# Kernel optimization log

Measured on AMD Instinct MI355X. Metric: run time of the kernel, lower is better.

The kernel has to match this reference:

```python
import jax, jax.numpy as jnp
import numpy as np

B, T, IN, H, C = 64, 4096, 128, 256, 128


def setup_inputs() -> dict:
    key = jax.random.key(0)
    ks = jax.random.split(key, 7)
    s_ih = 1.0 / np.sqrt(H)
    return {
        "x": jax.random.normal(ks[0], (B, T, IN), dtype=jnp.float32),
        "W_ih": jax.random.uniform(ks[1], (4 * H, IN), jnp.float32, -s_ih, s_ih),
        "W_hh": jax.random.uniform(ks[2], (4 * H, H), jnp.float32, -s_ih, s_ih),
        "b_ih": jax.random.uniform(ks[3], (4 * H,), jnp.float32, -s_ih, s_ih),
        "b_hh": jax.random.uniform(ks[4], (4 * H,), jnp.float32, -s_ih, s_ih),
        "fc_w": jax.random.uniform(ks[5], (C, H), jnp.float32, -s_ih, s_ih),
        "fc_b": jax.random.uniform(ks[6], (C,), jnp.float32, -s_ih, s_ih),
    }


def lstm_cell(x_t, h, c, W_ih, W_hh, b_ih, b_hh):
    # gates: [B, 4H] in PyTorch order i, f, g, o
    gates = x_t @ W_ih.T + b_ih + h @ W_hh.T + b_hh
    i, f, g, o = jnp.split(gates, 4, axis=-1)
    i = jax.nn.sigmoid(i)
    f = jax.nn.sigmoid(f)
    g = jnp.tanh(g)
    o = jax.nn.sigmoid(o)
    c_new = f * c + i * g
    h_new = o * jnp.tanh(c_new)
    return h_new, c_new


def reference(x, W_ih, W_hh, b_ih, b_hh, fc_w, fc_b):
    # Precompute input projections for all timesteps in one big GEMM.
    x_proj = jnp.einsum('bti,gi->tbg', x, W_ih) + b_ih  # [T, B, 4H]

    def step(carry, xp_t):
        h, c = carry
        # truncate_length=1: the torch code detaches (h, c) at EVERY step.
        # Forward math is unaffected by detach.
        h = jax.lax.stop_gradient(h)
        c = jax.lax.stop_gradient(c)
        gates = xp_t + h @ W_hh.T + b_hh
        i, f, g, o = jnp.split(gates, 4, axis=-1)
        c_new = jax.nn.sigmoid(f) * c + jax.nn.sigmoid(i) * jnp.tanh(g)
        h_new = jax.nn.sigmoid(o) * jnp.tanh(c_new)
        return (h_new, c_new), None

    h0 = jnp.zeros((x.shape[0], W_hh.shape[1]), dtype=x.dtype)
    c0 = jnp.zeros_like(h0)
    (h_t, _), _ = jax.lax.scan(step, (h0, c0), x_proj)
    return h_t @ fc_w.T + fc_b
```

## Files before the change

kernel.cpp:

```cpp
#include <hip/hip_runtime.h>

#define B_ 64
#define T_ 4096
#define IN_ 128
#define H_ 256
#define TPB 512

using u64 = unsigned long long;

static constexpr size_t HB2_BYTES = 2ull * B_ * H_ * sizeof(u64);

__device__ __forceinline__ float rdlane_f(float v, int k) {
    return __builtin_bit_cast(float, __builtin_amdgcn_readlane(__builtin_bit_cast(int, v), k));
}
__device__ __forceinline__ float fast_rcp(float x) { return __builtin_amdgcn_rcpf(x); }
__device__ __forceinline__ float fast_sigmoid(float x) {
    return fast_rcp(1.0f + __expf(-x));
}
__device__ __forceinline__ float fast_tanh(float x) {
    float ax = fabsf(x);
    float e  = __expf(-2.0f * ax);
    float t  = (1.0f - e) * fast_rcp(1.0f + e);
    return copysignf(t, x);
}
__device__ __forceinline__ u64 ld_agent(const u64* p) {
    return __hip_atomic_load(p, __ATOMIC_RELAXED, __HIP_MEMORY_SCOPE_AGENT);
}
__device__ __forceinline__ void st_agent(u64* p, u64 v) {
    __hip_atomic_store(p, v, __ATOMIC_RELAXED, __HIP_MEMORY_SCOPE_AGENT);
}

__global__ __launch_bounds__(TPB, 2) void lstm_persist(
    const float* __restrict__ x,
    const float* __restrict__ W_ih,
    const float* __restrict__ W_hh,
    const float* __restrict__ b_ih,
    const float* __restrict__ b_hh,
    const float* __restrict__ fc_w,
    const float* __restrict__ fc_b,
    float* __restrict__ out,
    u64* hb2)
{
    const int blk  = blockIdx.x;
    const int xcd  = blk & 7;
    const int m    = blk >> 3;
    const int s    = m & 3;
    const int b    = ((m >> 2) << 3) | xcd;
    const int tid  = threadIdx.x;
    const int lane = tid & 63;
    const int wave = tid >> 6;
    const int chunk = wave & 3;
    const int sub   = wave >> 2;
    const bool is_upd = (wave == s);

    const int row_base = s * 64 + lane;
    const int k_hh = chunk * 64 + sub * 32;
    const int k_ih = chunk * 32 + sub * 16;

    float w_hh[4][32];
    #pragma unroll
    for (int g = 0; g < 4; ++g) {
        const float4* src = (const float4*)(W_hh + (size_t)(g * 256 + row_base) * H_ + k_hh);
        #pragma unroll
        for (int q = 0; q < 8; ++q) {
            const float4 v = src[q];
            w_hh[g][q*4+0] = v.x; w_hh[g][q*4+1] = v.y;
            w_hh[g][q*4+2] = v.z; w_hh[g][q*4+3] = v.w;
        }
    }
    float w_ih[4][16];
    #pragma unroll
    for (int g = 0; g < 4; ++g) {
        const float4* src = (const float4*)(W_ih + (size_t)(g * 256 + row_base) * IN_ + k_ih);
        #pragma unroll
        for (int q = 0; q < 4; ++q) {
            const float4 v = src[q];
            w_ih[g][q*4+0] = v.x; w_ih[g][q*4+1] = v.y;
            w_ih[g][q*4+2] = v.z; w_ih[g][q*4+3] = v.w;
        }
    }
    float bias_[4] = {0.f, 0.f, 0.f, 0.f};
    if (is_upd) {
        #pragma unroll
        for (int g = 0; g < 4; ++g)
            bias_[g] = b_ih[g * 256 + row_base] + b_hh[g * 256 + row_base];
    }

    __shared__ float part[2][8][4][64];

    float h_own = 0.0f, c_own = 0.0f;

    const float* xb = x + (size_t)b * T_ * IN_;
    float vx = xb[k_ih + (lane & 15)];

    u64* const hb_b = hb2 + (size_t)b * 256;
    const u64* const poll0 = hb2 + (size_t)b * 256 + chunk * 64 + lane;

    for (int t = 0; t < T_; ++t) {
        const int p  = t & 1;
        const int pn = p ^ 1;
        float a0 = 0.f, a1 = 0.f, a2 = 0.f, a3 = 0.f;

        const int tn = (t + 1 < T_) ? t + 1 : t;
        const float vxn = xb[(size_t)tn * IN_ + k_ih + (lane & 15)];

        #pragma unroll
        for (int k = 0; k < 16; ++k) {
            const float xv = rdlane_f(vx, k);
            a0 = fmaf(xv, w_ih[0][k], a0);
            a1 = fmaf(xv, w_ih[1][k], a1);
            a2 = fmaf(xv, w_ih[2][k], a2);
            a3 = fmaf(xv, w_ih[3][k], a3);
        }
        vx = vxn;

        float vh;
        if (is_upd) {
            vh = h_own;
        } else {
            const u64* pp = poll0 + (size_t)p * (B_ * 256);
            u64 v = ld_agent(pp);
            const unsigned tv = (unsigned)t;
            while ((unsigned)(v >> 32) < tv) v = ld_agent(pp);
            vh = __builtin_bit_cast(float, (unsigned)v);
        }

        if (sub == 0) {
            #pragma unroll
            for (int k = 0; k < 32; ++k) {
                const float hv = rdlane_f(vh, k);
                a0 = fmaf(hv, w_hh[0][k], a0);
                a1 = fmaf(hv, w_hh[1][k], a1);
                a2 = fmaf(hv, w_hh[2][k], a2);
                a3 = fmaf(hv, w_hh[3][k], a3);
            }
        } else {
            #pragma unroll
            for (int k = 0; k < 32; ++k) {
                const float hv = rdlane_f(vh, 32 + k);
                a0 = fmaf(hv, w_hh[0][k], a0);
                a1 = fmaf(hv, w_hh[1][k], a1);
                a2 = fmaf(hv, w_hh[2][k], a2);
                a3 = fmaf(hv, w_hh[3][k], a3);
            }
        }

        part[p][wave][0][lane] = a0;
        part[p][wave][1][lane] = a1;
        part[p][wave][2][lane] = a2;
        part[p][wave][3][lane] = a3;
        __syncthreads();

        if (is_upd) {
            float gi = bias_[0], gf = bias_[1], gg = bias_[2], go = bias_[3];
            #pragma unroll
            for (int pc = 0; pc < 8; ++pc) {
                gi += part[p][pc][0][lane];
                gf += part[p][pc][1][lane];
                gg += part[p][pc][2][lane];
                go += part[p][pc][3][lane];
            }
            const float i_ = fast_sigmoid(gi);
            const float f_ = fast_sigmoid(gf);
            const float g_ = fast_tanh(gg);
            const float o_ = fast_sigmoid(go);
            c_own = fmaf(f_, c_own, i_ * g_);
            h_own = o_ * fast_tanh(c_own);
            const u64 pk = ((u64)(unsigned)(t + 1) << 32)
                         | (u64)__builtin_bit_cast(unsigned, h_own);
            st_agent(hb_b + (size_t)pn * (B_ * 256) + s * 64 + lane, pk);
        }
    }

    const u64* hT = hb2 + (size_t)(T_ & 1) * (B_ * 256) + (size_t)b * 256;
    const int c = s * 32 + (tid >> 4);
    const int q = tid & 15;
    float pacc = 0.0f;
    #pragma unroll
    for (int e = 0; e < 16; ++e) {
        u64 v;
        do { v = ld_agent(hT + q * 16 + e); } while ((unsigned)(v >> 32) < (unsigned)T_);
        pacc = fmaf(fc_w[(size_t)c * H_ + q * 16 + e],
                    __builtin_bit_cast(float, (unsigned)v), pacc);
    }
    pacc += __shfl_xor(pacc, 1);
    pacc += __shfl_xor(pacc, 2);
    pacc += __shfl_xor(pacc, 4);
    pacc += __shfl_xor(pacc, 8);
    if (q == 0) out[(size_t)b * 128 + c] = pacc + fc_b[c];
}

extern "C" void kernel_launch(void* const* d_in, const int* in_sizes, int n_in,
                              void* d_out, int out_size, void* d_ws, size_t ws_size,
                              hipStream_t stream) {
    const float* x    = (const float*)d_in[0];
    const float* W_ih = (const float*)d_in[1];
    const float* W_hh = (const float*)d_in[2];
    const float* b_ih = (const float*)d_in[3];
    const float* b_hh = (const float*)d_in[4];
    const float* fc_w = (const float*)d_in[5];
    const float* fc_b = (const float*)d_in[6];
    float* out = (float*)d_out;

    u64* hb2 = (u64*)d_ws;
    hipMemsetAsync(d_ws, 0, HB2_BYTES, stream);

    lstm_persist<<<B_ * 4, TPB, 0, stream>>>(x, W_ih, W_hh, b_ih, b_hh, fc_w, fc_b,
                                             out, hb2);
}
```

Measured before the change: 6.007 ms.

## Add dual-path hidden-state exchange with speculative slow load and sc0 fast polling

The updater now writes each new hidden value twice: a plain store to a fast buffer and an agent-scope store to a second slow buffer. Consumers issue a speculative agent-scope load from the slow buffer early in the step, overlapping it with the input projection. If that value is stale, they poll the fast buffer with inline-asm sc0 loads and fall back to the slow buffer after eight tries. The aim is to cut cross-block synchronisation latency per timestep. In exchange it doubles the store traffic, and it depends on plain stores and sc0 loads becoming visible across XCDs, which the memory model may not guarantee.

```diff
diff --git a/kernel.cpp b/kernel.cpp
--- a/kernel.cpp
+++ b/kernel.cpp
@@ -8,7 +8,8 @@
 
 using u64 = unsigned long long;
 
-static constexpr size_t HB2_BYTES = 2ull * B_ * H_ * sizeof(u64);
+static constexpr size_t HBUF_U64 = 2ull * B_ * H_;
+static constexpr size_t SLOW_OFF = HBUF_U64;
 
 __device__ __forceinline__ float rdlane_f(float v, int k) {
     return __builtin_bit_cast(float, __builtin_amdgcn_readlane(__builtin_bit_cast(int, v), k));
@@ -28,6 +29,15 @@
 }
 __device__ __forceinline__ void st_agent(u64* p, u64 v) {
     __hip_atomic_store(p, v, __ATOMIC_RELAXED, __HIP_MEMORY_SCOPE_AGENT);
+}
+__device__ __forceinline__ u64 ld_sc0(const u64* p) {
+    u64 r;
+    asm volatile("global_load_dwordx2 %0, %1, off sc0\n\ts_waitcnt vmcnt(0)"
+                 : "=v"(r) : "v"(p) : "memory");
+    return r;
+}
+__device__ __forceinline__ void st_plain(u64* p, u64 v) {
+    asm volatile("global_store_dwordx2 %0, %1, off" :: "v"(p), "v"(v) : "memory");
 }
 
 __global__ __launch_bounds__(TPB, 2) void lstm_persist(
@@ -39,7 +49,7 @@
     const float* __restrict__ fc_w,
     const float* __restrict__ fc_b,
     float* __restrict__ out,
-    u64* hb2)
+    u64* hb)
 {
     const int blk  = blockIdx.x;
     const int xcd  = blk & 7;
@@ -93,13 +103,19 @@
     const float* xb = x + (size_t)b * T_ * IN_;
     float vx = xb[k_ih + (lane & 15)];
 
-    u64* const hb_b = hb2 + (size_t)b * 256;
-    const u64* const poll0 = hb2 + (size_t)b * 256 + chunk * 64 + lane;
+    u64* const hb_b  = hb + (size_t)b * 256;
+    const u64* const poll0 = hb + (size_t)b * 256 + chunk * 64 + lane;
 
     for (int t = 0; t < T_; ++t) {
         const int p  = t & 1;
         const int pn = p ^ 1;
         float a0 = 0.f, a1 = 0.f, a2 = 0.f, a3 = 0.f;
+
+        const u64* pp_fast = poll0 + (size_t)p * (B_ * 256);
+        const u64* pp_slow = pp_fast + SLOW_OFF;
+
+        u64 vspec = 0;
+        if (!is_upd) vspec = ld_agent(pp_slow);
 
         const int tn = (t + 1 < T_) ? t + 1 : t;
         const float vxn = xb[(size_t)tn * IN_ + k_ih + (lane & 15)];
@@ -118,10 +134,19 @@
         if (is_upd) {
             vh = h_own;
         } else {
-            const u64* pp = poll0 + (size_t)p * (B_ * 256);
-            u64 v = ld_agent(pp);
+            u64 v = vspec;
             const unsigned tv = (unsigned)t;
-            while ((unsigned)(v >> 32) < tv) v = ld_agent(pp);
+            if ((unsigned)(v >> 32) < tv) {
+                int tries = 0;
+                for (;;) {
+                    v = ld_sc0(pp_fast);
+                    if ((unsigned)(v >> 32) >= tv) break;
+                    if (++tries >= 8) {
+                        u64 w = ld_agent(pp_slow);
+                        if ((unsigned)(w >> 32) >= tv) { v = w; break; }
+                    }
+                }
+            }
             vh = __builtin_bit_cast(float, (unsigned)v);
         }
 
@@ -168,11 +193,13 @@
             h_own = o_ * fast_tanh(c_own);
             const u64 pk = ((u64)(unsigned)(t + 1) << 32)
                          | (u64)__builtin_bit_cast(unsigned, h_own);
-            st_agent(hb_b + (size_t)pn * (B_ * 256) + s * 64 + lane, pk);
-        }
-    }
-
-    const u64* hT = hb2 + (size_t)(T_ & 1) * (B_ * 256) + (size_t)b * 256;
+            u64* dst = hb_b + (size_t)pn * (B_ * 256) + s * 64 + lane;
+            st_plain(dst, pk);
+            st_agent(dst + SLOW_OFF, pk);
+        }
+    }
+
+    const u64* hT = hb + SLOW_OFF + (size_t)(T_ & 1) * (B_ * 256) + (size_t)b * 256;
     const int c = s * 32 + (tid >> 4);
     const int q = tid & 15;
     float pacc = 0.0f;
@@ -202,9 +229,9 @@
     const float* fc_b = (const float*)d_in[6];
     float* out = (float*)d_out;
 
-    u64* hb2 = (u64*)d_ws;
-    hipMemsetAsync(d_ws, 0, HB2_BYTES, stream);
+    u64* hb = (u64*)d_ws;
+    hipMemsetAsync(d_ws, 0, 2ull * HBUF_U64 * sizeof(u64), stream);
 
     lstm_persist<<<B_ * 4, TPB, 0, stream>>>(x, W_ih, W_hh, b_ih, b_hh, fc_w, fc_b,
-                                             out, hb2);
-}
+                                             out, hb);
+}
```

Result: slower. 8.049 ms (+34.0%).

## Issue speculative h poll early, unroll timesteps by two, prefetch x two steps ahead

Applied to the files above, without the earlier changes.

Each timestep now issues the first poll of the shared hidden state before the input-projection FMAs, so the load latency overlaps with compute. The spin loop keeps two loads in flight at once. The loop is unrolled by two so x can be prefetched two steps ahead into alternating registers, and the bias is folded into the accumulator start. The shared partial-sum layout is transposed, and __syncthreads is replaced by an explicit lgkmcnt wait plus s_barrier. The extra in-flight loads add memory traffic and register pressure.

```diff
diff --git a/kernel.cpp b/kernel.cpp
--- a/kernel.cpp
+++ b/kernel.cpp
@@ -8,7 +8,8 @@
 
 using u64 = unsigned long long;
 
-static constexpr size_t HB2_BYTES = 2ull * B_ * H_ * sizeof(u64);
+static constexpr int HB_STRIDE = B_ * H_;
+static constexpr size_t HB_BYTES = 2ull * HB_STRIDE * sizeof(u64);
 
 __device__ __forceinline__ float rdlane_f(float v, int k) {
     return __builtin_bit_cast(float, __builtin_amdgcn_readlane(__builtin_bit_cast(int, v), k));
@@ -28,6 +29,10 @@
 }
 __device__ __forceinline__ void st_agent(u64* p, u64 v) {
     __hip_atomic_store(p, v, __ATOMIC_RELAXED, __HIP_MEMORY_SCOPE_AGENT);
+}
+__device__ __forceinline__ void barrier_lgkm() {
+    asm volatile("s_waitcnt lgkmcnt(0)" ::: "memory");
+    __builtin_amdgcn_s_barrier();
 }
 
 __global__ __launch_bounds__(TPB, 2) void lstm_persist(
@@ -39,7 +44,7 @@
     const float* __restrict__ fc_w,
     const float* __restrict__ fc_b,
     float* __restrict__ out,
-    u64* hb2)
+    u64* hb)
 {
     const int blk  = blockIdx.x;
     const int xcd  = blk & 7;
@@ -51,7 +56,7 @@
     const int wave = tid >> 6;
     const int chunk = wave & 3;
     const int sub   = wave >> 2;
-    const bool is_upd = (wave == s);
+    const bool is_upd = (chunk == s && sub == 0);
 
     const int row_base = s * 64 + lane;
     const int k_hh = chunk * 64 + sub * 32;
@@ -86,24 +91,25 @@
             bias_[g] = b_ih[g * 256 + row_base] + b_hh[g * 256 + row_base];
     }
 
-    __shared__ float part[2][8][4][64];
+    __shared__ float part[2][4][8][64];
 
     float h_own = 0.0f, c_own = 0.0f;
 
     const float* xb = x + (size_t)b * T_ * IN_;
-    float vx = xb[k_ih + (lane & 15)];
-
-    u64* const hb_b = hb2 + (size_t)b * 256;
-    const u64* const poll0 = hb2 + (size_t)b * 256 + chunk * 64 + lane;
-
-    for (int t = 0; t < T_; ++t) {
-        const int p  = t & 1;
+    float vx0 = xb[k_ih + (lane & 15)];
+    float vx1 = xb[IN_ + k_ih + (lane & 15)];
+
+    u64* const hstore = hb + (size_t)b * H_ + s * 64 + lane;
+    const u64* const poll0 = hb + (size_t)b * H_ + chunk * 64 + lane;
+
+    auto step = [&](const int t, const int p, const float vx, float& vx_slot) {
         const int pn = p ^ 1;
-        float a0 = 0.f, a1 = 0.f, a2 = 0.f, a3 = 0.f;
-
-        const int tn = (t + 1 < T_) ? t + 1 : t;
-        const float vxn = xb[(size_t)tn * IN_ + k_ih + (lane & 15)];
-
+        const u64* pp = poll0 + (size_t)p * HB_STRIDE;
+
+        u64 vspec = 0;
+        if (!is_upd) vspec = ld_agent(pp);
+
+        float a0 = bias_[0], a1 = bias_[1], a2 = bias_[2], a3 = bias_[3];
         #pragma unroll
         for (int k = 0; k < 16; ++k) {
             const float xv = rdlane_f(vx, k);
@@ -112,17 +118,29 @@
             a2 = fmaf(xv, w_ih[2][k], a2);
             a3 = fmaf(xv, w_ih[3][k], a3);
         }
-        vx = vxn;
 
         float vh;
         if (is_upd) {
             vh = h_own;
         } else {
-            const u64* pp = poll0 + (size_t)p * (B_ * 256);
-            u64 v = ld_agent(pp);
+            u64 v = vspec;
             const unsigned tv = (unsigned)t;
-            while ((unsigned)(v >> 32) < tv) v = ld_agent(pp);
+            if ((unsigned)(v >> 32) < tv) {
+                u64 vA = ld_agent(pp);
+                u64 vB = ld_agent(pp);
+                for (;;) {
+                    if ((unsigned)(vA >> 32) >= tv) { v = vA; break; }
+                    vA = ld_agent(pp);
+                    if ((unsigned)(vB >> 32) >= tv) { v = vB; break; }
+                    vB = ld_agent(pp);
+                }
+            }
             vh = __builtin_bit_cast(float, (unsigned)v);
+        }
+
+        {
+            const int tf = (t + 2 < T_) ? (t + 2) : (T_ - 1);
+            vx_slot = xb[(size_t)tf * IN_ + k_ih + (lane & 15)];
         }
 
         if (sub == 0) {
@@ -145,20 +163,21 @@
             }
         }
 
-        part[p][wave][0][lane] = a0;
-        part[p][wave][1][lane] = a1;
-        part[p][wave][2][lane] = a2;
-        part[p][wave][3][lane] = a3;
-        __syncthreads();
+        part[p][0][wave][lane] = a0;
+        part[p][1][wave][lane] = a1;
+        part[p][2][wave][lane] = a2;
+        part[p][3][wave][lane] = a3;
+
+        barrier_lgkm();
 
         if (is_upd) {
-            float gi = bias_[0], gf = bias_[1], gg = bias_[2], go = bias_[3];
+            float gi = 0.f, gf = 0.f, gg = 0.f, go = 0.f;
             #pragma unroll
-            for (int pc = 0; pc < 8; ++pc) {
-                gi += part[p][pc][0][lane];
-                gf += part[p][pc][1][lane];
-                gg += part[p][pc][2][lane];
-                go += part[p][pc][3][lane];
+            for (int w = 0; w < 8; ++w) {
+                gi += part[p][0][w][lane];
+                gf += part[p][1][w][lane];
+                gg += part[p][2][w][lane];
+                go += part[p][3][w][lane];
             }
             const float i_ = fast_sigmoid(gi);
             const float f_ = fast_sigmoid(gf);
@@ -168,11 +187,16 @@
             h_own = o_ * fast_tanh(c_own);
             const u64 pk = ((u64)(unsigned)(t + 1) << 32)
                          | (u64)__builtin_bit_cast(unsigned, h_own);
-            st_agent(hb_b + (size_t)pn * (B_ * 256) + s * 64 + lane, pk);
-        }
-    }
-
-    const u64* hT = hb2 + (size_t)(T_ & 1) * (B_ * 256) + (size_t)b * 256;
+            st_agent(hstore + (size_t)pn * HB_STRIDE, pk);
+        }
+    };
+
+    for (int t = 0; t < T_; t += 2) {
+        step(t,     0, vx0, vx0);
+        step(t + 1, 1, vx1, vx1);
+    }
+
+    const u64* hT = hb + (size_t)(T_ & 1) * HB_STRIDE + (size_t)b * H_;
     const int c = s * 32 + (tid >> 4);
     const int q = tid & 15;
     float pacc = 0.0f;
@@ -202,9 +226,9 @@
     const float* fc_b = (const float*)d_in[6];
     float* out = (float*)d_out;
 
-    u64* hb2 = (u64*)d_ws;
-    hipMemsetAsync(d_ws, 0, HB2_BYTES, stream);
+    u64* hb = (u64*)d_ws;
+    hipMemsetAsync(d_ws, 0, HB_BYTES, stream);
 
     lstm_persist<<<B_ * 4, TPB, 0, stream>>>(x, W_ih, W_hh, b_ih, b_hh, fc_w, fc_b,
-                                             out, hb2);
-}
+                                             out, hb);
+}
```

Result: slower. 6.603 ms (+9.9%).

## Pack LSTM weights and hidden state to fp16 with dot2 and halve wave count

Applied to the files above, without the earlier changes.

Weights and the exchanged hidden state are converted to packed fp16 and multiplied with fdot2, which halves the register footprint and the bytes moved per step. Each block now uses 4 waves instead of 8, and two h values are packed per 64-bit message to cut global polling traffic. The block's own slice is read from LDS rather than from global memory. Block-to-XCD mapping is simplified, and fp16 rounding of weights and h adds numerical error over 4096 recurrent steps.

```diff
diff --git a/kernel.cpp b/kernel.cpp
--- a/kernel.cpp
+++ b/kernel.cpp
@@ -4,15 +4,15 @@
 #define T_ 4096
 #define IN_ 128
 #define H_ 256
-#define TPB 512
+#define TPB 256
 
 using u64 = unsigned long long;
-
-static constexpr size_t HB2_BYTES = 2ull * B_ * H_ * sizeof(u64);
-
-__device__ __forceinline__ float rdlane_f(float v, int k) {
-    return __builtin_bit_cast(float, __builtin_amdgcn_readlane(__builtin_bit_cast(int, v), k));
-}
+using u32 = unsigned int;
+typedef _Float16 h2_t __attribute__((ext_vector_type(2)));
+
+static constexpr size_t PSTR    = (size_t)B_ * 4 * 32;
+static constexpr size_t GHB_U64 = 2 * PSTR;
+
 __device__ __forceinline__ float fast_rcp(float x) { return __builtin_amdgcn_rcpf(x); }
 __device__ __forceinline__ float fast_sigmoid(float x) {
     return fast_rcp(1.0f + __expf(-x));
@@ -29,8 +29,21 @@
 __device__ __forceinline__ void st_agent(u64* p, u64 v) {
     __hip_atomic_store(p, v, __ATOMIC_RELAXED, __HIP_MEMORY_SCOPE_AGENT);
 }
-
-__global__ __launch_bounds__(TPB, 2) void lstm_persist(
+__device__ __forceinline__ u64 ld_lds(const u64* p) {
+    return __hip_atomic_load(p, __ATOMIC_RELAXED, __HIP_MEMORY_SCOPE_WORKGROUP);
+}
+__device__ __forceinline__ void st_lds(u64* p, u64 v) {
+    __hip_atomic_store(p, v, __ATOMIC_RELAXED, __HIP_MEMORY_SCOPE_WORKGROUP);
+}
+__device__ __forceinline__ void barrier_lgkm() {
+    asm volatile("s_waitcnt lgkmcnt(0)" ::: "memory");
+    __builtin_amdgcn_s_barrier();
+}
+__device__ __forceinline__ u32 pk16(float a, float b) {
+    return __builtin_bit_cast(u32, __builtin_amdgcn_cvt_pkrtz(a, b));
+}
+
+__global__ __launch_bounds__(TPB, 1) void lstm_persist(
     const float* __restrict__ x,
     const float* __restrict__ W_ih,
     const float* __restrict__ W_hh,
@@ -39,155 +52,169 @@
     const float* __restrict__ fc_w,
     const float* __restrict__ fc_b,
     float* __restrict__ out,
-    u64* hb2)
+    u64* ghb)
 {
     const int blk  = blockIdx.x;
-    const int xcd  = blk & 7;
-    const int m    = blk >> 3;
-    const int s    = m & 3;
-    const int b    = ((m >> 2) << 3) | xcd;
+    const int b    = blk >> 2;
+    const int s    = blk & 3;
     const int tid  = threadIdx.x;
     const int lane = tid & 63;
-    const int wave = tid >> 6;
-    const int chunk = wave & 3;
-    const int sub   = wave >> 2;
-    const bool is_upd = (wave == s);
-
-    const int row_base = s * 64 + lane;
-    const int k_hh = chunk * 64 + sub * 32;
-    const int k_ih = chunk * 32 + sub * 16;
-
-    float w_hh[4][32];
+    const int w    = tid >> 6;
+    const int wS   = __builtin_amdgcn_readfirstlane(w);
+    const bool is_upd = (w == s);
+
+    const int r0 = (s == 0) ? 1 : 0;
+    const int r1 = (s <= 1) ? 2 : 1;
+    const int r2 = (s <= 2) ? 3 : 2;
+
+    u32 whh[4][32];
     #pragma unroll
     for (int g = 0; g < 4; ++g) {
-        const float4* src = (const float4*)(W_hh + (size_t)(g * 256 + row_base) * H_ + k_hh);
-        #pragma unroll
-        for (int q = 0; q < 8; ++q) {
-            const float4 v = src[q];
-            w_hh[g][q*4+0] = v.x; w_hh[g][q*4+1] = v.y;
-            w_hh[g][q*4+2] = v.z; w_hh[g][q*4+3] = v.w;
-        }
-    }
-    float w_ih[4][16];
+        const float* rowp = W_hh + (size_t)(g * 256 + s * 64 + lane) * H_;
+        #pragma unroll
+        for (int c = 0; c < 4; ++c)
+            #pragma unroll
+            for (int pp = 0; pp < 8; ++pp) {
+                const float2 v = *(const float2*)(rowp + c * 64 + w * 16 + 2 * pp);
+                whh[g][c * 8 + pp] = pk16(v.x, v.y);
+            }
+    }
+    u32 wih[4][16];
     #pragma unroll
     for (int g = 0; g < 4; ++g) {
-        const float4* src = (const float4*)(W_ih + (size_t)(g * 256 + row_base) * IN_ + k_ih);
-        #pragma unroll
-        for (int q = 0; q < 4; ++q) {
-            const float4 v = src[q];
-            w_ih[g][q*4+0] = v.x; w_ih[g][q*4+1] = v.y;
-            w_ih[g][q*4+2] = v.z; w_ih[g][q*4+3] = v.w;
+        const float* rowp = W_ih + (size_t)(g * 256 + s * 64 + lane) * IN_;
+        #pragma unroll
+        for (int pp = 0; pp < 16; ++pp) {
+            const float2 v = *(const float2*)(rowp + w * 32 + 2 * pp);
+            wih[g][pp] = pk16(v.x, v.y);
         }
     }
     float bias_[4] = {0.f, 0.f, 0.f, 0.f};
     if (is_upd) {
         #pragma unroll
         for (int g = 0; g < 4; ++g)
-            bias_[g] = b_ih[g * 256 + row_base] + b_hh[g * 256 + row_base];
-    }
-
-    __shared__ float part[2][8][4][64];
-
-    float h_own = 0.0f, c_own = 0.0f;
+            bias_[g] = b_ih[g * 256 + s * 64 + lane] + b_hh[g * 256 + s * 64 + lane];
+    }
+
+    __shared__ float part[2][4][4][64];
+    __shared__ u64 hlds[2][32];
+    if (tid < 32) { hlds[0][tid] = 0; hlds[1][tid] = 0; }
+    __syncthreads();
+
+    float c_own = 0.0f;
 
     const float* xb = x + (size_t)b * T_ * IN_;
-    float vx = xb[k_ih + (lane & 15)];
-
-    u64* const hb_b = hb2 + (size_t)b * 256;
-    const u64* const poll0 = hb2 + (size_t)b * 256 + chunk * 64 + lane;
+    float2 vx0, vx1;
+    if (lane < 16) {
+        vx0 = *(const float2*)(xb + w * 32 + 2 * lane);
+        vx1 = *(const float2*)(xb + IN_ + w * 32 + 2 * lane);
+    }
+
+    const u64* A0 = ghb + ((size_t)b * 4 + (lane < 32 ? r0 : r1)) * 32 + (lane & 31);
+    const u64* B0 = ghb + ((size_t)b * 4 + r2) * 32 + (lane & 31);
+    u64* const S0 = ghb + ((size_t)b * 4 + s) * 32 + (lane & 31);
 
     for (int t = 0; t < T_; ++t) {
         const int p  = t & 1;
         const int pn = p ^ 1;
-        float a0 = 0.f, a1 = 0.f, a2 = 0.f, a3 = 0.f;
-
-        const int tn = (t + 1 < T_) ? t + 1 : t;
-        const float vxn = xb[(size_t)tn * IN_ + k_ih + (lane & 15)];
-
-        #pragma unroll
-        for (int k = 0; k < 16; ++k) {
-            const float xv = rdlane_f(vx, k);
-            a0 = fmaf(xv, w_ih[0][k], a0);
-            a1 = fmaf(xv, w_ih[1][k], a1);
-            a2 = fmaf(xv, w_ih[2][k], a2);
-            a3 = fmaf(xv, w_ih[3][k], a3);
-        }
-        vx = vxn;
-
-        float vh;
+        const u32 tv = (u32)t;
+        const u64* pA = A0 + (size_t)p * PSTR;
+        const u64* pB = B0 + (size_t)p * PSTR;
+
+        u64 vA = ld_agent(pA);
+        u64 vB = ld_agent(pB);
+        u64 vL = ld_lds(&hlds[p][lane & 31]);
+
+        const u32 xpk = pk16(vx0.x, vx0.y);
+        float a0 = bias_[0], a1 = bias_[1], a2 = bias_[2], a3 = bias_[3];
+        #pragma unroll
+        for (int pp = 0; pp < 16; ++pp) {
+            const h2_t xp = __builtin_bit_cast(h2_t, __builtin_amdgcn_readlane(xpk, pp));
+            a0 = __builtin_amdgcn_fdot2(__builtin_bit_cast(h2_t, wih[0][pp]), xp, a0, false);
+            a1 = __builtin_amdgcn_fdot2(__builtin_bit_cast(h2_t, wih[1][pp]), xp, a1, false);
+            a2 = __builtin_amdgcn_fdot2(__builtin_bit_cast(h2_t, wih[2][pp]), xp, a2, false);
+            a3 = __builtin_amdgcn_fdot2(__builtin_bit_cast(h2_t, wih[3][pp]), xp, a3, false);
+        }
+
+        while ((u32)(vA >> 32) < tv || (u32)(vB >> 32) < tv) {
+            vA = ld_agent(pA);
+            vB = ld_agent(pB);
+        }
+        while ((u32)(vL >> 32) < tv) vL = ld_lds(&hlds[p][lane & 31]);
+
+        vx0 = vx1;
+        {
+            const int tf = (t + 2 < T_) ? (t + 2) : (T_ - 1);
+            if (lane < 16) vx1 = *(const float2*)(xb + (size_t)tf * IN_ + w * 32 + 2 * lane);
+        }
+
+        const u32 loA = (u32)vA, loB = (u32)vB, loL = (u32)vL;
+        auto mac8 = [&](int cbase, u32 reg, int lofs) {
+            #pragma unroll
+            for (int pp = 0; pp < 8; ++pp) {
+                const h2_t hp = __builtin_bit_cast(h2_t,
+                    __builtin_amdgcn_readlane(reg, lofs + wS * 8 + pp));
+                a0 = __builtin_amdgcn_fdot2(__builtin_bit_cast(h2_t, whh[0][cbase + pp]), hp, a0, false);
+                a1 = __builtin_amdgcn_fdot2(__builtin_bit_cast(h2_t, whh[1][cbase + pp]), hp, a1, false);
+                a2 = __builtin_amdgcn_fdot2(__builtin_bit_cast(h2_t, whh[2][cbase + pp]), hp, a2, false);
+                a3 = __builtin_amdgcn_fdot2(__builtin_bit_cast(h2_t, whh[3][cbase + pp]), hp, a3, false);
+            }
+        };
+        mac8(s  * 8, loL, 0);
+        mac8(r0 * 8, loA, 0);
+        mac8(r1 * 8, loA, 32);
+        mac8(r2 * 8, loB, 0);
+
+        part[p][w][0][lane] = a0;
+        part[p][w][1][lane] = a1;
+        part[p][w][2][lane] = a2;
+        part[p][w][3][lane] = a3;
+
+        barrier_lgkm();
+
         if (is_upd) {
-            vh = h_own;
-        } else {
-            const u64* pp = poll0 + (size_t)p * (B_ * 256);
-            u64 v = ld_agent(pp);
-            const unsigned tv = (unsigned)t;
-            while ((unsigned)(v >> 32) < tv) v = ld_agent(pp);
-            vh = __builtin_bit_cast(float, (unsigned)v);
-        }
-
-        if (sub == 0) {
-            #pragma unroll
-            for (int k = 0; k < 32; ++k) {
-                const float hv = rdlane_f(vh, k);
-                a0 = fmaf(hv, w_hh[0][k], a0);
-                a1 = fmaf(hv, w_hh[1][k], a1);
-                a2 = fmaf(hv, w_hh[2][k], a2);
-                a3 = fmaf(hv, w_hh[3][k], a3);
-            }
-        } else {
-            #pragma unroll
-            for (int k = 0; k < 32; ++k) {
-                const float hv = rdlane_f(vh, 32 + k);
-                a0 = fmaf(hv, w_hh[0][k], a0);
-                a1 = fmaf(hv, w_hh[1][k], a1);
-                a2 = fmaf(hv, w_hh[2][k], a2);
-                a3 = fmaf(hv, w_hh[3][k], a3);
-            }
-        }
-
-        part[p][wave][0][lane] = a0;
-        part[p][wave][1][lane] = a1;
-        part[p][wave][2][lane] = a2;
-        part[p][wave][3][lane] = a3;
-        __syncthreads();
-
-        if (is_upd) {
-            float gi = bias_[0], gf = bias_[1], gg = bias_[2], go = bias_[3];
-            #pragma unroll
-            for (int pc = 0; pc < 8; ++pc) {
-                gi += part[p][pc][0][lane];
-                gf += part[p][pc][1][lane];
-                gg += part[p][pc][2][lane];
-                go += part[p][pc][3][lane];
-            }
+            const float gi = part[p][0][0][lane] + part[p][1][0][lane]
+                           + part[p][2][0][lane] + part[p][3][0][lane];
+            const float gf = part[p][0][1][lane] + part[p][1][1][lane]
+                           + part[p][2][1][lane] + part[p][3][1][lane];
+            const float gg = part[p][0][2][lane] + part[p][1][2][lane]
+                           + part[p][2][2][lane] + part[p][3][2][lane];
+            const float go = part[p][0][3][lane] + part[p][1][3][lane]
+                           + part[p][2][3][lane] + part[p][3][3][lane];
             const float i_ = fast_sigmoid(gi);
             const float f_ = fast_sigmoid(gf);
             const float g_ = fast_tanh(gg);
             const float o_ = fast_sigmoid(go);
             c_own = fmaf(f_, c_own, i_ * g_);
-            h_own = o_ * fast_tanh(c_own);
-            const u64 pk = ((u64)(unsigned)(t + 1) << 32)
-                         | (u64)__builtin_bit_cast(unsigned, h_own);
-            st_agent(hb_b + (size_t)pn * (B_ * 256) + s * 64 + lane, pk);
-        }
-    }
-
-    const u64* hT = hb2 + (size_t)(T_ & 1) * (B_ * 256) + (size_t)b * 256;
-    const int c = s * 32 + (tid >> 4);
-    const int q = tid & 15;
-    float pacc = 0.0f;
+            const float h_ = o_ * fast_tanh(c_own);
+            const float he = __shfl(h_, 2 * (lane & 31));
+            const float ho = __shfl(h_, 2 * (lane & 31) + 1);
+            const u64 msg = ((u64)(u32)(t + 1) << 32) | (u64)pk16(he, ho);
+            if (lane < 32) {
+                st_agent(S0 + (size_t)pn * PSTR, msg);
+                st_lds(&hlds[pn][lane], msg);
+            }
+        }
+    }
+
+    const u64* hT = ghb + (size_t)b * 4 * 32;
+    const int c = s * 32 + (tid >> 3);
+    const int q = tid & 7;
+    float acc = 0.0f;
     #pragma unroll
-    for (int e = 0; e < 16; ++e) {
+    for (int e = 0; e < 32; ++e) {
+        const int k = q * 32 + e;
+        const u64* ps = hT + (k >> 6) * 32 + ((k >> 1) & 31);
         u64 v;
-        do { v = ld_agent(hT + q * 16 + e); } while ((unsigned)(v >> 32) < (unsigned)T_);
-        pacc = fmaf(fc_w[(size_t)c * H_ + q * 16 + e],
-                    __builtin_bit_cast(float, (unsigned)v), pacc);
-    }
-    pacc += __shfl_xor(pacc, 1);
-    pacc += __shfl_xor(pacc, 2);
-    pacc += __shfl_xor(pacc, 4);
-    pacc += __shfl_xor(pacc, 8);
-    if (q == 0) out[(size_t)b * 128 + c] = pacc + fc_b[c];
+        do { v = ld_agent(ps); } while ((u32)(v >> 32) < (u32)T_);
+        const h2_t h2 = __builtin_bit_cast(h2_t, (u32)v);
+        const float hv = (float)((k & 1) ? h2.y : h2.x);
+        acc = fmaf(fc_w[(size_t)c * H_ + k], hv, acc);
+    }
+    acc += __shfl_xor(acc, 1);
+    acc += __shfl_xor(acc, 2);
+    acc += __shfl_xor(acc, 4);
+    if (q == 0) out[(size_t)b * 128 + c] = acc + fc_b[c];
 }
 
 extern "C" void kernel_launch(void* const* d_in, const int* in_sizes, int n_in,
@@ -202,9 +229,9 @@
     const float* fc_b = (const float*)d_in[6];
     float* out = (float*)d_out;
 
-    u64* hb2 = (u64*)d_ws;
-    hipMemsetAsync(d_ws, 0, HB2_BYTES, stream);
+    u64* ghb = (u64*)d_ws;
+    hipMemsetAsync(d_ws, 0, GHB_U64 * sizeof(u64), stream);
 
     lstm_persist<<<B_ * 4, TPB, 0, stream>>>(x, W_ih, W_hh, b_ih, b_hh, fc_w, fc_b,
-                                             out, hb2);
-}
+                                             out, ghb);
+}
```

Result: slower. 23.26 ms (+287.2%).
